# Performance work log

Measured on AMD Instinct MI355X. Metric: run time of the kernel, lower is better.

Reference implementation:

```python
import jax, jax.numpy as jnp
import numpy as np

HIDDEN = 2048
NUM_HEADS = 16
NUM_KV_HEADS = 8
HEAD_DIM = 128
Q_SIZE = NUM_HEADS * HEAD_DIM          # 2048
KV_SIZE = NUM_KV_HEADS * HEAD_DIM      # 1024
ROPE_THETA = 1000000.0
RMS_EPS = 1e-6
SCALE = HEAD_DIM ** -0.5


def setup_inputs() -> dict:
    key = jax.random.key(0)
    k1, k2, k3 = jax.random.split(key, 3)
    T = 4096
    positions = jnp.arange(T, dtype=jnp.int64) if jax.config.jax_enable_x64 else jnp.arange(T, dtype=jnp.int32)
    hidden_states = jax.random.normal(k1, (T, HIDDEN), dtype=jnp.float32)
    qkv_w = jax.random.normal(k2, (Q_SIZE + 2 * KV_SIZE, HIDDEN), dtype=jnp.float32) * 0.02
    o_w = jax.random.normal(k3, (HIDDEN, Q_SIZE), dtype=jnp.float32) * 0.02
    q_norm_w = jnp.ones((HEAD_DIM,), dtype=jnp.float32)
    k_norm_w = jnp.ones((HEAD_DIM,), dtype=jnp.float32)
    return {
        "hidden_states": hidden_states,
        "qkv_w": qkv_w,
        "q_norm_w": q_norm_w,
        "k_norm_w": k_norm_w,
        "o_w": o_w,
        "positions": positions,
    }


def _rms_norm(x, w, eps=RMS_EPS):
    # per-head RMSNorm over last dim (head_dim)
    var = jnp.mean(jnp.square(x), axis=-1, keepdims=True)
    return x * jax.lax.rsqrt(var + eps) * w


def _rope(x, positions):
    # neox-style (rotate-half) RoPE. x: [T, H, D], positions: [T]
    D = x.shape[-1]
    inv_freq = 1.0 / (ROPE_THETA ** (jnp.arange(0, D, 2, dtype=jnp.float32) / D))  # [D/2]
    freqs = positions.astype(jnp.float32)[:, None] * inv_freq                      # [T, D/2]
    cos = jnp.cos(freqs)[:, None, :]  # [T, 1, D/2]
    sin = jnp.sin(freqs)[:, None, :]
    x1, x2 = x[..., : D // 2], x[..., D // 2 :]
    return jnp.concatenate([x1 * cos - x2 * sin, x2 * cos + x1 * sin], axis=-1)


def reference(hidden_states, qkv_w, q_norm_w, k_norm_w, o_w, positions):
    T = hidden_states.shape[0]
    qkv = hidden_states @ qkv_w.T                                   # [T, Q+2KV]
    q = qkv[:, :Q_SIZE].reshape(T, NUM_HEADS, HEAD_DIM)
    k = qkv[:, Q_SIZE : Q_SIZE + KV_SIZE].reshape(T, NUM_KV_HEADS, HEAD_DIM)
    v = qkv[:, Q_SIZE + KV_SIZE :].reshape(T, NUM_KV_HEADS, HEAD_DIM)

    # attention_bias=False path: per-head QK RMSNorm
    q = _rms_norm(q, q_norm_w)
    k = _rms_norm(k, k_norm_w)

    q = _rope(q, positions)
    k = _rope(k, positions)

    # GQA: expand KV heads to query heads
    rep = NUM_HEADS // NUM_KV_HEADS
    k = jnp.repeat(k, rep, axis=1)   # [T, H, D]
    v = jnp.repeat(v, rep, axis=1)

    scores = jnp.einsum("qhd,khd->hqk", q, k) * SCALE               # [H, T, T]
    causal = positions[:, None] >= positions[None, :]               # [T, T]
    scores = jnp.where(causal[None], scores, jnp.finfo(scores.dtype).min)
    probs = jax.nn.softmax(scores, axis=-1)
    attn = jnp.einsum("hqk,khd->qhd", probs, v)                     # [T, H, D]
    return attn.reshape(T, Q_SIZE) @ o_w.T                          # [T, HIDDEN]
```

## Files before the change

kernel.cpp:

```cpp
#include <hip/hip_runtime.h>
#include <hip/hip_bf16.h>
#include <math.h>


typedef __bf16 bf16;
typedef __bf16 bf16x4 __attribute__((ext_vector_type(4)));
typedef __bf16 bf16x8 __attribute__((ext_vector_type(8)));
typedef float  f32x4  __attribute__((ext_vector_type(4)));

__device__ __forceinline__ f32x4 mfma16(bf16x8 a, bf16x8 b, f32x4 c) {
  return __builtin_amdgcn_mfma_f32_16x16x32_bf16(a, b, c, 0, 0, 0);
}

__device__ __forceinline__ void mfma16x16_chain4(const bf16x4& a0, const bf16x4& a1,
                                                 const bf16x4& a2, const bf16x4& a3,
                                                 const bf16x4& b0, const bf16x4& b1,
                                                 const bf16x4& b2, const bf16x4& b3,
                                                 f32x4& c) {
  asm volatile(
      "s_nop 2\n\t"
      "v_mfma_f32_16x16x16_bf16 %0, %1, %5, %0\n\t"
      "v_mfma_f32_16x16x16_bf16 %0, %2, %6, %0\n\t"
      "v_mfma_f32_16x16x16_bf16 %0, %3, %7, %0\n\t"
      "v_mfma_f32_16x16x16_bf16 %0, %4, %8, %0"
      : "+v"(c)
      : "v"(a0), "v"(a1), "v"(a2), "v"(a3),
        "v"(b0), "v"(b1), "v"(b2), "v"(b3));
}

__device__ __forceinline__ void gload_lds16(const bf16* g, bf16* l) {
  __builtin_amdgcn_global_load_lds(
      (const __attribute__((address_space(1))) unsigned int*)g,
      (__attribute__((address_space(3))) unsigned int*)l, 16, 0, 0);
}

__device__ __forceinline__ void store_c(float* p, float v) { *p = v; }
__device__ __forceinline__ void store_c(bf16* p, float v) { *p = (bf16)v; }

__global__ __launch_bounds__(256) void cast_bf16(const float* __restrict__ s,
                                                 bf16* __restrict__ d) {
  int i = blockIdx.x * 256 + threadIdx.x;
  float4 a = reinterpret_cast<const float4*>(s)[i * 2];
  float4 b = reinterpret_cast<const float4*>(s)[i * 2 + 1];
  bf16x8 v = {(bf16)a.x, (bf16)a.y, (bf16)a.z, (bf16)a.w,
              (bf16)b.x, (bf16)b.y, (bf16)b.z, (bf16)b.w};
  reinterpret_cast<bf16x8*>(d)[i] = v;
}

__global__ __launch_bounds__(512, 2) void gemm256(const bf16* __restrict__ A,
                                                  const bf16* __restrict__ B,
                                                  bf16* __restrict__ C,
                                                  int M, int N, int K) {
  __shared__ __align__(16) bf16 As[3][256 * 32];
  __shared__ __align__(16) bf16 Bs[3][256 * 32];

  const int tid  = threadIdx.x;
  const int lane = tid & 63;
  const int wid  = tid >> 6;
  const int quad = lane >> 4, l16 = lane & 15;
  const int wr = wid >> 2, wc = wid & 3;

  const int nbx = N >> 8;
  const int nwg = (M >> 8) * nbx;
  const int cpx = nwg >> 3;
  const int swz = (blockIdx.x & 7) * cpx + (blockIdx.x >> 3);
  const int m0 = (swz / nbx) << 8;
  const int n0 = (swz % nbx) << 8;

  const int srow = tid >> 2, scol = (tid & 3) * 8;
  const bf16* aSrc0 = &A[(size_t)(m0 + srow) * K + scol];
  const bf16* aSrc1 = &A[(size_t)(m0 + 128 + srow) * K + scol];
  const bf16* bSrc0 = &B[(size_t)(n0 + srow) * K + scol];
  const bf16* bSrc1 = &B[(size_t)(n0 + 128 + srow) * K + scol];

  const f32x4 zero = {0.f, 0.f, 0.f, 0.f};
  f32x4 acc[8][4];
#pragma unroll
  for (int i = 0; i < 8; ++i)
#pragma unroll
    for (int j = 0; j < 4; ++j) acc[i][j] = zero;

  const int NT = K >> 5;

  {
    gload_lds16(aSrc0, &As[0][tid * 8]);
    gload_lds16(aSrc1, &As[0][4096 + tid * 8]);
    gload_lds16(bSrc0, &Bs[0][tid * 8]);
    gload_lds16(bSrc1, &Bs[0][4096 + tid * 8]);
    gload_lds16(aSrc0 + 32, &As[1][tid * 8]);
    gload_lds16(aSrc1 + 32, &As[1][4096 + tid * 8]);
    gload_lds16(bSrc0 + 32, &Bs[1][tid * 8]);
    gload_lds16(bSrc1 + 32, &Bs[1][4096 + tid * 8]);
  }

  int bufC = 0;
  for (int t = 0; t < NT; ++t) {
    if (t == NT - 1) {
      asm volatile("s_waitcnt vmcnt(0)" ::: "memory");
    } else {
      asm volatile("s_waitcnt vmcnt(4)" ::: "memory");
    }
    __builtin_amdgcn_s_barrier();
    __builtin_amdgcn_sched_barrier(0);

    if (t + 2 < NT) {
      int bs = bufC + 2; if (bs >= 3) bs -= 3;
      const int k0 = (t + 2) * 32;
      gload_lds16(aSrc0 + k0, &As[bs][tid * 8]);
      gload_lds16(aSrc1 + k0, &As[bs][4096 + tid * 8]);
      gload_lds16(bSrc0 + k0, &Bs[bs][tid * 8]);
      gload_lds16(bSrc1 + k0, &Bs[bs][4096 + tid * 8]);
    }

    const bf16* AsL = As[bufC];
    const bf16* BsL = Bs[bufC];
    bf16x8 af[8], bfv[4];
#pragma unroll
    for (int fm = 0; fm < 8; ++fm)
      af[fm] = *reinterpret_cast<const bf16x8*>(
          &AsL[(wr * 128 + fm * 16 + l16) * 32 + quad * 8]);
#pragma unroll
    for (int fn = 0; fn < 4; ++fn)
      bfv[fn] = *reinterpret_cast<const bf16x8*>(
          &BsL[(wc * 64 + fn * 16 + l16) * 32 + quad * 8]);
#pragma unroll
    for (int fm = 0; fm < 8; ++fm)
#pragma unroll
      for (int fn = 0; fn < 4; ++fn)
        acc[fm][fn] = mfma16(af[fm], bfv[fn], acc[fm][fn]);

    bufC = bufC + 1 == 3 ? 0 : bufC + 1;
  }

#pragma unroll
  for (int fm = 0; fm < 8; ++fm)
#pragma unroll
    for (int fn = 0; fn < 4; ++fn)
#pragma unroll
      for (int r = 0; r < 4; ++r) {
        int row = m0 + wr * 128 + fm * 16 + quad * 4 + r;
        int col = n0 + wc * 64 + fn * 16 + l16;
        C[(size_t)row * N + col] = (bf16)acc[fm][fn][r];
      }
}

__device__ __forceinline__ void gemm_step(const bf16* AsL, const bf16* BsL,
                                          int wm, int wn, int l16, int quad,
                                          f32x4 (&acc)[4][4]) {
  bf16x8 af[4], bfr[4];
#pragma unroll
  for (int i = 0; i < 4; ++i)
    af[i] = *reinterpret_cast<const bf16x8*>(&AsL[(wm + i * 16 + l16) * 32 + quad * 8]);
#pragma unroll
  for (int j = 0; j < 4; ++j)
    bfr[j] = *reinterpret_cast<const bf16x8*>(&BsL[(wn + j * 16 + l16) * 32 + quad * 8]);
#pragma unroll
  for (int i = 0; i < 4; ++i)
#pragma unroll
    for (int j = 0; j < 4; ++j)
      acc[i][j] = mfma16(af[i], bfr[j], acc[i][j]);
}

template <typename TC>
__global__ __launch_bounds__(256, 4) void gemm_bt(const bf16* __restrict__ A,
                                                  const bf16* __restrict__ B,
                                                  TC* __restrict__ C,
                                                  int M, int N, int K) {
  __shared__ __align__(16) bf16 As[2][128 * 32];
  __shared__ __align__(16) bf16 Bs[2][128 * 32];

  const int tid  = threadIdx.x;
  const int wave = tid >> 6, lane = tid & 63;
  const int quad = lane >> 4, l16 = lane & 15;
  const int wm = (wave >> 1) * 64, wn = (wave & 1) * 64;
  const int n0 = blockIdx.x * 128, m0 = blockIdx.y * 128;

  const int r0 = tid >> 2;
  const int c0 = (tid & 3) * 8;
  const size_t aBase = (size_t)(m0 + r0) * K + c0;
  const size_t bBase = (size_t)(n0 + r0) * K + c0;
  const size_t rowK64 = (size_t)64 * K;

  const f32x4 zero = {0.f, 0.f, 0.f, 0.f};
  f32x4 acc[4][4];
#pragma unroll
  for (int i = 0; i < 4; ++i)
#pragma unroll
    for (int j = 0; j < 4; ++j) acc[i][j] = zero;

  gload_lds16(&A[aBase],          &As[0][tid * 8]);
  gload_lds16(&A[aBase + rowK64], &As[0][2048 + tid * 8]);
  gload_lds16(&B[bBase],          &Bs[0][tid * 8]);
  gload_lds16(&B[bBase + rowK64], &Bs[0][2048 + tid * 8]);
  __syncthreads();

  int cur = 0;
  for (int k0 = 32; k0 < K; k0 += 32) {
    const int nb = cur ^ 1;
    gload_lds16(&A[aBase + k0],          &As[nb][tid * 8]);
    gload_lds16(&A[aBase + rowK64 + k0], &As[nb][2048 + tid * 8]);
    gload_lds16(&B[bBase + k0],          &Bs[nb][tid * 8]);
    gload_lds16(&B[bBase + rowK64 + k0], &Bs[nb][2048 + tid * 8]);

    gemm_step(As[cur], Bs[cur], wm, wn, l16, quad, acc);

    __syncthreads();
    cur = nb;
  }
  gemm_step(As[cur], Bs[cur], wm, wn, l16, quad, acc);

#pragma unroll
  for (int i = 0; i < 4; ++i)
#pragma unroll
    for (int j = 0; j < 4; ++j)
#pragma unroll
      for (int r = 0; r < 4; ++r) {
        int row = m0 + wm + i * 16 + quad * 4 + r;
        int col = n0 + wn + j * 16 + l16;
        store_c(&C[(size_t)row * N + col], acc[i][j][r]);
      }
}

__global__ __launch_bounds__(256) void norm_rope(const bf16* __restrict__ qkv,
                                                 const float* __restrict__ qw,
                                                 const float* __restrict__ kw,
                                                 const int* __restrict__ pos,
                                                 bf16* __restrict__ qn,
                                                 bf16* __restrict__ kn) {
  const int t = blockIdx.x;
  const int wv = threadIdx.x >> 6, l = threadIdx.x & 63;

  float inv = exp2f((float)l * (-19.93156856932417f / 64.0f));
  float fr = (float)pos[t] * inv;
  float sn, cs;
  sincosf(fr, &sn, &cs);
  const float qw1 = qw[l], qw2 = qw[l + 64];
  const float kw1 = kw[l], kw2 = kw[l + 64];
  const size_t rowb = (size_t)t * 4096;

#pragma unroll
  for (int i = 0; i < 6; ++i) {
    const int h = wv * 6 + i;
    const bool isq = h < 16;
    const int col = isq ? h * 128 : 2048 + (h - 16) * 128;
    float x1 = (float)qkv[rowb + col + l];
    float x2 = (float)qkv[rowb + col + l + 64];
    float ss = x1 * x1 + x2 * x2;
#pragma unroll
    for (int o = 32; o >= 1; o >>= 1) ss += __shfl_xor(ss, o);
    float rms = rsqrtf(ss * (1.0f / 128.0f) + 1e-6f);
    float w1 = isq ? qw1 : kw1, w2 = isq ? qw2 : kw2;
    float xn1 = x1 * rms * w1, xn2 = x2 * rms * w2;
    float o1 = xn1 * cs - xn2 * sn;
    float o2 = xn2 * cs + xn1 * sn;
    if (isq) {
      qn[(size_t)t * 2048 + h * 128 + l] = (bf16)o1;
      qn[(size_t)t * 2048 + h * 128 + l + 64] = (bf16)o2;
    } else {
      kn[(size_t)t * 1024 + (h - 16) * 128 + l] = (bf16)o1;
      kn[(size_t)t * 1024 + (h - 16) * 128 + l + 64] = (bf16)o2;
    }
  }
}

__global__ __launch_bounds__(256) void transpose_v(const bf16* __restrict__ qkv,
                                                   bf16* __restrict__ vt) {
  __shared__ __align__(16) bf16 tile[128 * 72];
  const int t0 = blockIdx.x * 64, kvh = blockIdx.y;
  const int tid = threadIdx.x;
#pragma unroll
  for (int it = 0; it < 2; ++it) {
    int linear = it * 4096 + tid * 16;
    int r = linear >> 7, c = linear & 127;
    union { uint4 v; bf16 e[8]; } u0, u1;
    u0.v = *reinterpret_cast<const uint4*>(
        &qkv[(size_t)(t0 + r) * 4096 + 3072 + kvh * 128 + c]);
    u1.v = *reinterpret_cast<const uint4*>(
        &qkv[(size_t)(t0 + r) * 4096 + 3072 + kvh * 128 + c + 8]);
#pragma unroll
    for (int j = 0; j < 8; ++j) tile[(c + j) * 72 + r] = u0.e[j];
#pragma unroll
    for (int j = 0; j < 8; ++j) tile[(c + 8 + j) * 72 + r] = u1.e[j];
  }
  __syncthreads();
#pragma unroll
  for (int it = 0; it < 4; ++it) {
    int linear = it * 2048 + tid * 8;
    int d = linear >> 6, c = linear & 63;
    uint4 v = *reinterpret_cast<const uint4*>(&tile[d * 72 + c]);
    *reinterpret_cast<uint4*>(&vt[(size_t)(kvh * 128 + d) * 4096 + t0 + c]) = v;
  }
}

__global__ __launch_bounds__(256, 2) void attn(const bf16* __restrict__ q,
                                               const bf16* __restrict__ k,
                                               const bf16* __restrict__ vt,
                                               bf16* __restrict__ out) {
  __shared__ __align__(16) bf16 Ks[2][64 * 128];
  __shared__ __align__(16) bf16 Vs[2][128 * 64];

  const int head = blockIdx.y, kvh = head >> 1;
  const int bx = blockIdx.x;

  const int tid = threadIdx.x;
  const int wave = tid >> 6, lane = tid & 63;
  const int quad = lane >> 4, l16 = lane & 15;
  const float cExp = 0.08838834764831845f * 1.4426950408889634f;
  const f32x4 zero = {0.f, 0.f, 0.f, 0.f};

  int kSrc[4], vSrc[4];
#pragma unroll
  for (int it = 0; it < 4; ++it) {
    int r = (wave * 4 + it) * 4 + (lane >> 4);
    kSrc[it] = r * 1024 + kvh * 128 + (((lane & 15) ^ (r & 7)) << 3);
    int d = (wave * 4 + it) * 8 + (lane >> 3);
    vSrc[it] = (kvh * 128 + d) * 4096 + (((lane & 7) ^ (lane >> 3)) << 3);
  }

  const int kswz = (l16 & 7) << 3;
  int koff[4], voff[4];
#pragma unroll
  for (int s = 0; s < 4; ++s) {
    koff[s] = (s * 32 + quad * 8) ^ kswz;
    voff[s] = (s * 16 + quad * 4) ^ kswz;
  }

#pragma unroll
  for (int it = 0; it < 4; ++it) {
    gload_lds16(&k[kSrc[it]], &Ks[0][(wave * 4 + it) * 512]);
    gload_lds16(&vt[vSrc[it]], &Vs[0][(wave * 4 + it) * 512]);
  }
  int cur = 0;

#pragma unroll
  for (int phase = 0; phase < 2; ++phase) {
    const int qt = phase == 0 ? bx : 63 - bx;
    const int q0 = qt * 64;
    const int kend = q0 + 64;
    const int qrow = q0 + wave * 16 + l16;

    bf16x8 qf[4];
#pragma unroll
    for (int s = 0; s < 4; ++s)
      qf[s] = *reinterpret_cast<const bf16x8*>(
          &q[(size_t)qrow * 2048 + head * 128 + s * 32 + quad * 8]);

    f32x4 o_acc[8];
#pragma unroll
    for (int dt = 0; dt < 8; ++dt) o_acc[dt] = zero;
    float m_i = -3.0e38f, l_i = 0.f;

    for (int k0 = 0; k0 < kend; k0 += 64) {
      __syncthreads();

      int nk0 = -1;
      if (k0 + 64 < kend)     nk0 = k0 + 64;
      else if (phase == 0)    nk0 = 0;
      if (nk0 >= 0) {
#pragma unroll
        for (int it = 0; it < 4; ++it) {
          gload_lds16(&k[kSrc[it] + nk0 * 1024],
                      &Ks[cur ^ 1][(wave * 4 + it) * 512]);
          gload_lds16(&vt[vSrc[it] + nk0],
                      &Vs[cur ^ 1][(wave * 4 + it) * 512]);
        }
      }

      const bf16* KsL = Ks[cur];
      const bf16* VsL = Vs[cur];

      f32x4 s_acc[4];
      __builtin_amdgcn_s_setprio(1);
#pragma unroll
      for (int mt = 0; mt < 4; ++mt) {
        bf16x8 kf[4];
#pragma unroll
        for (int ks = 0; ks < 4; ++ks)
          kf[ks] = *reinterpret_cast<const bf16x8*>(
              &KsL[(mt * 16 + l16) * 128 + koff[ks]]);
        f32x4 sa = zero;
#pragma unroll
        for (int ks = 0; ks < 4; ++ks) sa = mfma16(kf[ks], qf[ks], sa);
        s_acc[mt] = sa;
      }
      __builtin_amdgcn_s_setprio(0);

      if (k0 == q0) {
        int tq = wave * 16 + l16;
#pragma unroll
        for (int mt = 0; mt < 4; ++mt)
#pragma unroll
          for (int r = 0; r < 4; ++r) {
            int tk = mt * 16 + quad * 4 + r;
            if (tk > tq) s_acc[mt][r] = -3.0e38f;
          }
      }

      {
        float mx = -3.0e38f;
#pragma unroll
        for (int mt = 0; mt < 4; ++mt)
#pragma unroll
          for (int r = 0; r < 4; ++r) mx = fmaxf(mx, s_acc[mt][r]);
        mx = fmaxf(mx, __shfl_xor(mx, 16));
        mx = fmaxf(mx, __shfl_xor(mx, 32));
        if (!__all((mx - m_i) * cExp <= 8.0f)) {
          float mn = fmaxf(m_i, mx);
          float al = exp2f((m_i - mn) * cExp);
          m_i = mn;
          l_i *= al;
#pragma unroll
          for (int dt = 0; dt < 8; ++dt)
#pragma unroll
            for (int r = 0; r < 4; ++r) o_acc[dt][r] *= al;
        }
        float nmc = -m_i * cExp;
        float rs = 0.f;
#pragma unroll
        for (int mt = 0; mt < 4; ++mt)
#pragma unroll
          for (int r = 0; r < 4; ++r) {
            float pe = exp2f(fmaf(s_acc[mt][r], cExp, nmc));
            s_acc[mt][r] = pe;
            rs += pe;
          }
        rs += __shfl_xor(rs, 16);
        rs += __shfl_xor(rs, 32);
        l_i += rs;
      }

      bf16x4 pb[4];
#pragma unroll
      for (int mt = 0; mt < 4; ++mt) {
        bf16x4 t;
#pragma unroll
        for (int r = 0; r < 4; ++r) t[r] = (bf16)s_acc[mt][r];
        pb[mt] = t;
      }

      __builtin_amdgcn_s_setprio(1);
#pragma unroll
      for (int dt = 0; dt < 8; ++dt) {
        const bf16* vrow = &VsL[(dt * 16 + l16) * 64];
        bf16x4 va0 = *reinterpret_cast<const bf16x4*>(&vrow[voff[0]]);
        bf16x4 va1 = *reinterpret_cast<const bf16x4*>(&vrow[voff[1]]);
        bf16x4 va2 = *reinterpret_cast<const bf16x4*>(&vrow[voff[2]]);
        bf16x4 va3 = *reinterpret_cast<const bf16x4*>(&vrow[voff[3]]);
        mfma16x16_chain4(va0, va1, va2, va3, pb[0], pb[1], pb[2], pb[3],
                         o_acc[dt]);
      }
      __builtin_amdgcn_s_setprio(0);
      cur ^= 1;
    }

    float rl = __builtin_amdgcn_rcpf(l_i);
#pragma unroll
    for (int dt = 0; dt < 8; ++dt) {
      bf16x4 ov;
#pragma unroll
      for (int r = 0; r < 4; ++r) ov[r] = (bf16)(o_acc[dt][r] * rl);
      *reinterpret_cast<bf16x4*>(
          &out[(size_t)qrow * 2048 + head * 128 + dt * 16 + quad * 4]) = ov;
    }
  }
}

extern "C" void kernel_launch(void* const* d_in, const int* in_sizes, int n_in,
                              void* d_out, int out_size, void* d_ws, size_t ws_size,
                              hipStream_t stream) {
  const float* hidden = (const float*)d_in[0];
  const float* qkv_w  = (const float*)d_in[1];
  const float* qnw    = (const float*)d_in[2];
  const float* knw    = (const float*)d_in[3];
  const float* o_w    = (const float*)d_in[4];
  const int*   pos    = (const int*)d_in[5];

  bf16* qkv = (bf16*)d_ws;
  bf16* qn  = qkv + (size_t)4096 * 4096;
  bf16* kn  = qn  + (size_t)4096 * 2048;
  bf16* vt  = kn  + (size_t)4096 * 1024;
  bf16* ao  = vt  + (size_t)1024 * 4096;
  bf16* hb  = ao;
  bf16* wq  = kn;
  bf16* wo  = qn;
  float* out = (float*)d_out;

  cast_bf16<<<4096, 256, 0, stream>>>(hidden, hb);
  cast_bf16<<<4096, 256, 0, stream>>>(qkv_w, wq);
  gemm256<<<256, 512, 0, stream>>>(hb, wq, qkv, 4096, 4096, 2048);
  norm_rope<<<4096, 256, 0, stream>>>(qkv, qnw, knw, pos, qn, kn);
  transpose_v<<<dim3(64, 8), 256, 0, stream>>>(qkv, vt);
  attn<<<dim3(32, 16), 256, 0, stream>>>(qn, kn, vt, ao);
  cast_bf16<<<2048, 256, 0, stream>>>(o_w, wo);
  gemm_bt<<<dim3(16, 32), 256, 0, stream>>>(ao, wo, out, 4096, 2048, 2048);
}
```

Baseline: 417.4 us.

## Drop LDS double buffering and paired q-tiles for single-tile blocks at higher occupancy

The attention kernel no longer pairs a short and a long causal query tile per block. Each block now handles one query tile, and heavier tiles are launched first. The double-buffered K/V LDS staging becomes a single buffer loaded synchronously each iteration, which halves LDS use and lets launch bounds target 4 blocks per CU. The intent is to raise occupancy and rely on inter-block overlap to hide load latency. The trade-off is losing in-block prefetch overlap and adding a second barrier per iteration.

```diff
diff --git a/kernel.cpp b/kernel.cpp
--- a/kernel.cpp
+++ b/kernel.cpp
@@ -292,15 +292,17 @@
   }
 }
 
-__global__ __launch_bounds__(256, 2) void attn(const bf16* __restrict__ q,
+__global__ __launch_bounds__(256, 4) void attn(const bf16* __restrict__ q,
                                                const bf16* __restrict__ k,
                                                const bf16* __restrict__ vt,
                                                bf16* __restrict__ out) {
-  __shared__ __align__(16) bf16 Ks[2][64 * 128];
-  __shared__ __align__(16) bf16 Vs[2][128 * 64];
+  __shared__ __align__(16) bf16 Ks[64 * 128];
+  __shared__ __align__(16) bf16 Vs[128 * 64];
 
   const int head = blockIdx.y, kvh = head >> 1;
-  const int bx = blockIdx.x;
+  const int qt = 63 - (int)blockIdx.x;
+  const int q0 = qt * 64;
+  const int kend = q0 + 64;
 
   const int tid = threadIdx.x;
   const int wave = tid >> 6, lane = tid & 63;
@@ -325,143 +327,120 @@
     voff[s] = (s * 16 + quad * 4) ^ kswz;
   }
 
-#pragma unroll
-  for (int it = 0; it < 4; ++it) {
-    gload_lds16(&k[kSrc[it]], &Ks[0][(wave * 4 + it) * 512]);
-    gload_lds16(&vt[vSrc[it]], &Vs[0][(wave * 4 + it) * 512]);
-  }
-  int cur = 0;
-
-#pragma unroll
-  for (int phase = 0; phase < 2; ++phase) {
-    const int qt = phase == 0 ? bx : 63 - bx;
-    const int q0 = qt * 64;
-    const int kend = q0 + 64;
-    const int qrow = q0 + wave * 16 + l16;
-
-    bf16x8 qf[4];
-#pragma unroll
-    for (int s = 0; s < 4; ++s)
-      qf[s] = *reinterpret_cast<const bf16x8*>(
-          &q[(size_t)qrow * 2048 + head * 128 + s * 32 + quad * 8]);
-
-    f32x4 o_acc[8];
-#pragma unroll
-    for (int dt = 0; dt < 8; ++dt) o_acc[dt] = zero;
-    float m_i = -3.0e38f, l_i = 0.f;
-
-    for (int k0 = 0; k0 < kend; k0 += 64) {
-      __syncthreads();
-
-      int nk0 = -1;
-      if (k0 + 64 < kend)     nk0 = k0 + 64;
-      else if (phase == 0)    nk0 = 0;
-      if (nk0 >= 0) {
-#pragma unroll
-        for (int it = 0; it < 4; ++it) {
-          gload_lds16(&k[kSrc[it] + nk0 * 1024],
-                      &Ks[cur ^ 1][(wave * 4 + it) * 512]);
-          gload_lds16(&vt[vSrc[it] + nk0],
-                      &Vs[cur ^ 1][(wave * 4 + it) * 512]);
+  const int qrow = q0 + wave * 16 + l16;
+
+  bf16x8 qf[4];
+#pragma unroll
+  for (int s = 0; s < 4; ++s)
+    qf[s] = *reinterpret_cast<const bf16x8*>(
+        &q[(size_t)qrow * 2048 + head * 128 + s * 32 + quad * 8]);
+
+  f32x4 o_acc[8];
+#pragma unroll
+  for (int dt = 0; dt < 8; ++dt) o_acc[dt] = zero;
+  float m_i = -3.0e38f, l_i = 0.f;
+
+  for (int k0 = 0; k0 < kend; k0 += 64) {
+#pragma unroll
+    for (int it = 0; it < 4; ++it) {
+      gload_lds16(&k[kSrc[it] + k0 * 1024], &Ks[(wave * 4 + it) * 512]);
+      gload_lds16(&vt[vSrc[it] + k0],       &Vs[(wave * 4 + it) * 512]);
+    }
+    __syncthreads();
+
+    f32x4 s_acc[4];
+    __builtin_amdgcn_s_setprio(1);
+#pragma unroll
+    for (int mt = 0; mt < 4; ++mt) {
+      bf16x8 kf[4];
+#pragma unroll
+      for (int ks = 0; ks < 4; ++ks)
+        kf[ks] = *reinterpret_cast<const bf16x8*>(
+            &Ks[(mt * 16 + l16) * 128 + koff[ks]]);
+      f32x4 sa = zero;
+#pragma unroll
+      for (int ks = 0; ks < 4; ++ks) sa = mfma16(kf[ks], qf[ks], sa);
+      s_acc[mt] = sa;
+    }
+    __builtin_amdgcn_s_setprio(0);
+
+    if (k0 == q0) {
+      int tq = wave * 16 + l16;
+#pragma unroll
+      for (int mt = 0; mt < 4; ++mt)
+#pragma unroll
+        for (int r = 0; r < 4; ++r) {
+          int tk = mt * 16 + quad * 4 + r;
+          if (tk > tq) s_acc[mt][r] = -3.0e38f;
         }
+    }
+
+    {
+      float mx = -3.0e38f;
+#pragma unroll
+      for (int mt = 0; mt < 4; ++mt)
+#pragma unroll
+        for (int r = 0; r < 4; ++r) mx = fmaxf(mx, s_acc[mt][r]);
+      mx = fmaxf(mx, __shfl_xor(mx, 16));
+      mx = fmaxf(mx, __shfl_xor(mx, 32));
+      if (!__all((mx - m_i) * cExp <= 8.0f)) {
+        float mn = fmaxf(m_i, mx);
+        float al = exp2f((m_i - mn) * cExp);
+        m_i = mn;
+        l_i *= al;
+#pragma unroll
+        for (int dt = 0; dt < 8; ++dt)
+#pragma unroll
+          for (int r = 0; r < 4; ++r) o_acc[dt][r] *= al;
       }
-
-      const bf16* KsL = Ks[cur];
-      const bf16* VsL = Vs[cur];
-
-      f32x4 s_acc[4];
-      __builtin_amdgcn_s_setprio(1);
-#pragma unroll
-      for (int mt = 0; mt < 4; ++mt) {
-        bf16x8 kf[4];
-#pragma unroll
-        for (int ks = 0; ks < 4; ++ks)
-          kf[ks] = *reinterpret_cast<const bf16x8*>(
-              &KsL[(mt * 16 + l16) * 128 + koff[ks]]);
-        f32x4 sa = zero;
-#pragma unroll
-        for (int ks = 0; ks < 4; ++ks) sa = mfma16(kf[ks], qf[ks], sa);
-        s_acc[mt] = sa;
-      }
-      __builtin_amdgcn_s_setprio(0);
-
-      if (k0 == q0) {
-        int tq = wave * 16 + l16;
-#pragma unroll
-        for (int mt = 0; mt < 4; ++mt)
-#pragma unroll
-          for (int r = 0; r < 4; ++r) {
-            int tk = mt * 16 + quad * 4 + r;
-            if (tk > tq) s_acc[mt][r] = -3.0e38f;
-          }
-      }
-
-      {
-        float mx = -3.0e38f;
-#pragma unroll
-        for (int mt = 0; mt < 4; ++mt)
-#pragma unroll
-          for (int r = 0; r < 4; ++r) mx = fmaxf(mx, s_acc[mt][r]);
-        mx = fmaxf(mx, __shfl_xor(mx, 16));
-        mx = fmaxf(mx, __shfl_xor(mx, 32));
-        if (!__all((mx - m_i) * cExp <= 8.0f)) {
-          float mn = fmaxf(m_i, mx);
-          float al = exp2f((m_i - mn) * cExp);
-          m_i = mn;
-          l_i *= al;
-#pragma unroll
-          for (int dt = 0; dt < 8; ++dt)
-#pragma unroll
-            for (int r = 0; r < 4; ++r) o_acc[dt][r] *= al;
+      float nmc = -m_i * cExp;
+      float rs = 0.f;
+#pragma unroll
+      for (int mt = 0; mt < 4; ++mt)
+#pragma unroll
+        for (int r = 0; r < 4; ++r) {
+          float pe = exp2f(fmaf(s_acc[mt][r], cExp, nmc));
+          s_acc[mt][r] = pe;
+          rs += pe;
         }
-        float nmc = -m_i * cExp;
-        float rs = 0.f;
-#pragma unroll
-        for (int mt = 0; mt < 4; ++mt)
-#pragma unroll
-          for (int r = 0; r < 4; ++r) {
-            float pe = exp2f(fmaf(s_acc[mt][r], cExp, nmc));
-            s_acc[mt][r] = pe;
-            rs += pe;
-          }
-        rs += __shfl_xor(rs, 16);
-        rs += __shfl_xor(rs, 32);
-        l_i += rs;
-      }
-
-      bf16x4 pb[4];
-#pragma unroll
-      for (int mt = 0; mt < 4; ++mt) {
-        bf16x4 t;
-#pragma unroll
-        for (int r = 0; r < 4; ++r) t[r] = (bf16)s_acc[mt][r];
-        pb[mt] = t;
-      }
-
-      __builtin_amdgcn_s_setprio(1);
-#pragma unroll
-      for (int dt = 0; dt < 8; ++dt) {
-        const bf16* vrow = &VsL[(dt * 16 + l16) * 64];
-        bf16x4 va0 = *reinterpret_cast<const bf16x4*>(&vrow[voff[0]]);
-        bf16x4 va1 = *reinterpret_cast<const bf16x4*>(&vrow[voff[1]]);
-        bf16x4 va2 = *reinterpret_cast<const bf16x4*>(&vrow[voff[2]]);
-        bf16x4 va3 = *reinterpret_cast<const bf16x4*>(&vrow[voff[3]]);
-        mfma16x16_chain4(va0, va1, va2, va3, pb[0], pb[1], pb[2], pb[3],
-                         o_acc[dt]);
-      }
-      __builtin_amdgcn_s_setprio(0);
-      cur ^= 1;
-    }
-
-    float rl = __builtin_amdgcn_rcpf(l_i);
+      rs += __shfl_xor(rs, 16);
+      rs += __shfl_xor(rs, 32);
+      l_i += rs;
+    }
+
+    bf16x4 pb[4];
+#pragma unroll
+    for (int mt = 0; mt < 4; ++mt) {
+      bf16x4 t;
+#pragma unroll
+      for (int r = 0; r < 4; ++r) t[r] = (bf16)s_acc[mt][r];
+      pb[mt] = t;
+    }
+
+    __builtin_amdgcn_s_setprio(1);
 #pragma unroll
     for (int dt = 0; dt < 8; ++dt) {
-      bf16x4 ov;
-#pragma unroll
-      for (int r = 0; r < 4; ++r) ov[r] = (bf16)(o_acc[dt][r] * rl);
-      *reinterpret_cast<bf16x4*>(
-          &out[(size_t)qrow * 2048 + head * 128 + dt * 16 + quad * 4]) = ov;
-    }
+      const bf16* vrow = &Vs[(dt * 16 + l16) * 64];
+      bf16x4 va0 = *reinterpret_cast<const bf16x4*>(&vrow[voff[0]]);
+      bf16x4 va1 = *reinterpret_cast<const bf16x4*>(&vrow[voff[1]]);
+      bf16x4 va2 = *reinterpret_cast<const bf16x4*>(&vrow[voff[2]]);
+      bf16x4 va3 = *reinterpret_cast<const bf16x4*>(&vrow[voff[3]]);
+      mfma16x16_chain4(va0, va1, va2, va3, pb[0], pb[1], pb[2], pb[3],
+                       o_acc[dt]);
+    }
+    __builtin_amdgcn_s_setprio(0);
+
+    __syncthreads();
+  }
+
+  float rl = __builtin_amdgcn_rcpf(l_i);
+#pragma unroll
+  for (int dt = 0; dt < 8; ++dt) {
+    bf16x4 ov;
+#pragma unroll
+    for (int r = 0; r < 4; ++r) ov[r] = (bf16)(o_acc[dt][r] * rl);
+    *reinterpret_cast<bf16x4*>(
+        &out[(size_t)qrow * 2048 + head * 128 + dt * 16 + quad * 4]) = ov;
   }
 }
 
@@ -490,7 +469,7 @@
   gemm256<<<256, 512, 0, stream>>>(hb, wq, qkv, 4096, 4096, 2048);
   norm_rope<<<4096, 256, 0, stream>>>(qkv, qnw, knw, pos, qn, kn);
   transpose_v<<<dim3(64, 8), 256, 0, stream>>>(qkv, vt);
-  attn<<<dim3(32, 16), 256, 0, stream>>>(qn, kn, vt, ao);
+  attn<<<dim3(64, 16), 256, 0, stream>>>(qn, kn, vt, ao);
   cast_bf16<<<2048, 256, 0, stream>>>(o_w, wo);
   gemm_bt<<<dim3(16, 32), 256, 0, stream>>>(ao, wo, out, 4096, 2048, 2048);
 }
```

Measured after the change: 474.0 us. +13.5%, slower.
